# Optimization experiments

Measured on AMD Instinct MI355X. Metric: run time of the kernel, lower is better.

Reference implementation:

```python
import jax, jax.numpy as jnp
import numpy as np

LOSS_WEIGHT = 1.0
EPS = 1e-12  # numerical floor under the sqrt (module's eps)


def setup_inputs() -> dict:
    key = jax.random.key(0)
    k1, k2 = jax.random.split(key)
    N, P1, P2, D = 16, 4096, 4096, 2
    point_set_1 = jax.random.normal(k1, (N, P1, D), dtype=jnp.float32)
    point_set_2 = jax.random.normal(k2, (N, P2, D), dtype=jnp.float32)
    return {"point_set_1": point_set_1, "point_set_2": point_set_2}


def _chamfer_per_object(x, y):
    # x: [N, P1, 2], y: [N, P2, 2]
    # Pairwise squared L2 via expansion |x|^2 + |y|^2 - 2<x,y> (avoids [N,P1,P2,2] diff tensor)
    x2 = jnp.sum(x * x, axis=-1)                       # [N, P1]
    y2 = jnp.sum(y * y, axis=-1)                       # [N, P2]
    xy = jnp.einsum('npd,nqd->npq', x, y)              # [N, P1, P2]
    C = jnp.sqrt(jnp.clip(x2[:, :, None] + y2[:, None, :] - 2.0 * xy, EPS))  # [N, P1, P2]
    d1 = jnp.min(C, axis=-1).mean(axis=-1)             # min over P2, mean over P1 -> [N]
    d2 = jnp.min(C, axis=-2).mean(axis=-1)             # min over P1, mean over P2 -> [N]
    return 0.5 * (d1 + d2)                             # [N]


def reference(point_set_1, point_set_2):
    # Vectorized form of the per-object Python loop:
    # each object's chamfer (reduction='mean' over a batch of 1 == identity)
    # is masked by (set_2.sum() >= 0), summed, and divided by n_obj.
    cost = _chamfer_per_object(point_set_1, point_set_2)                 # [N]
    m = (jnp.sum(point_set_2, axis=(-1, -2)) >= 0).astype(cost.dtype)    # [N]
    return jnp.mean(cost * m) * LOSS_WEIGHT                              # scalar
```

## Files before the change

kernel.cpp:

```cpp
#include <hip/hip_runtime.h>
#include <math.h>

typedef float f32x2 __attribute__((ext_vector_type(2)));

#define N_OBJ 16
#define P 4096
#define BLOCK 256
#define R 8
#define ROWS_PER_BLOCK (BLOCK * R)
#define ROWBLOCKS (P / ROWS_PER_BLOCK)
#define CQ 16
#define QCHUNK (P / CQ)
#define JP (QCHUNK / 2)
#define EPSF 1e-12f
#define GRID_MAIN (2 * N_OBJ * ROWBLOCKS * CQ)

#define RED_ROWS 1024
#define RED_SLICES (P / RED_ROWS)
#define GRID_RED (2 * N_OBJ * RED_SLICES)


__device__ __forceinline__ float wave_sum(float s) {
#pragma unroll
    for (int off = 32; off > 0; off >>= 1)
        s += __shfl_xor(s, off, 64);
    return s;
}

__global__ __launch_bounds__(BLOCK) void k_main(const float* __restrict__ s1,
                                                const float* __restrict__ s2,
                                                float* __restrict__ pmin,
                                                unsigned* __restrict__ maskws) {
    const int per_pass = N_OBJ * ROWBLOCKS * CQ;
    int bid  = blockIdx.x;
    int tid  = threadIdx.x;
    int pass = bid / per_pass;
    int idx  = bid % per_pass;
    int n    = idx / (ROWBLOCKS * CQ);
    int rem  = idx % (ROWBLOCKS * CQ);
    int rb   = rem / CQ;
    int cq   = rem % CQ;

    __shared__ float4 lds[JP];
    __shared__ float wpart[BLOCK / 64];

    const float* T = (pass == 0) ? s1 : s2;
    const float* S = (pass == 0) ? s2 : s1;

    if (tid < JP) {
        int q = cq * QCHUNK + 2 * tid;
        float4 v = ((const float4*)S)[(n * P + q) >> 1];
        lds[tid] = make_float4(v.x, v.z, v.y, v.w);
    }

    f32x2 a0s[R], a1s[R];
    float c[R], m[R];
    int rbase = rb * ROWS_PER_BLOCK;
#pragma unroll
    for (int k = 0; k < R; k++) {
        int r = rbase + k * BLOCK + tid;
        float2 x = ((const float2*)T)[n * P + r];
        float a0 = -2.0f * x.x, a1 = -2.0f * x.y;
        a0s[k] = (f32x2){a0, a0};
        a1s[k] = (f32x2){a1, a1};
        c[k]   = fmaf(x.x, x.x, x.y * x.y);
        m[k]   = INFINITY;
    }

    {
        const float4* v2 = (const float4*)s2;
        float s = 0.0f;
#pragma unroll
        for (int k = 0; k < 8; k++) {
            float4 v = v2[n * 2048 + k * BLOCK + tid];
            s += (v.x + v.y) + (v.z + v.w);
        }
        s = wave_sum(s);
        if ((tid & 63) == 0) wpart[tid >> 6] = s;
    }
    __syncthreads();
    float total = (wpart[0] + wpart[1]) + (wpart[2] + wpart[3]);
    unsigned live = (total >= 0.0f) ? 1u : 0u;
    if (pass == 0 && rem == 0 && tid == 0) maskws[n] = live;
    if (!live) return;

#pragma unroll 4
    for (int jp = 0; jp < JP; jp++) {
        float4 v = lds[jp];
        f32x2 y0 = {v.x, v.y};
        f32x2 y1 = {v.z, v.w};
        f32x2 y2 = y0 * y0 + y1 * y1;
#pragma unroll
        for (int k = 0; k < R; k++) {
            f32x2 t = a1s[k] * y1 + y2;
            f32x2 d = a0s[k] * y0 + t;
            m[k] = fminf(fminf(d.x, d.y), m[k]);
        }
    }

    float* outp = pmin + ((size_t)((pass * N_OBJ + n) * CQ + cq)) * P
                + rbase + tid;
#pragma unroll
    for (int k = 0; k < R; k++) {
        outp[k * BLOCK] = fmaxf(m[k] + c[k], EPSF);
    }
}

__global__ __launch_bounds__(BLOCK) void k_red(const float* __restrict__ pmin,
                                               const unsigned* __restrict__ maskws,
                                               float* __restrict__ out) {
    int bid = blockIdx.x;
    int tid = threadIdx.x;
    int pn  = bid / RED_SLICES;
    int rs  = bid % RED_SLICES;
    int n   = pn & (N_OBJ - 1);
    __shared__ float wpart[BLOCK / 64];

    if (maskws[n] == 0u) return;

    const float* base = pmin + (size_t)pn * CQ * P + rs * RED_ROWS + 4 * tid;
    float4 mn = make_float4(INFINITY, INFINITY, INFINITY, INFINITY);
#pragma unroll
    for (int cq = 0; cq < CQ; cq++) {
        float4 v = *(const float4*)(base + (size_t)cq * P);
        mn.x = fminf(mn.x, v.x);
        mn.y = fminf(mn.y, v.y);
        mn.z = fminf(mn.z, v.z);
        mn.w = fminf(mn.w, v.w);
    }
    float s = (sqrtf(mn.x) + sqrtf(mn.y)) + (sqrtf(mn.z) + sqrtf(mn.w));
    s = wave_sum(s);
    if ((tid & 63) == 0) wpart[tid >> 6] = s;
    __syncthreads();
    if (tid == 0) {
        float sum = (wpart[0] + wpart[1]) + (wpart[2] + wpart[3]);
        atomicAdd(out, sum * (0.5f / (float)P / (float)N_OBJ));
    }
}

extern "C" void kernel_launch(void* const* d_in, const int* in_sizes, int n_in,
                              void* d_out, int out_size, void* d_ws, size_t ws_size,
                              hipStream_t stream) {
    const float* s1 = (const float*)d_in[0];
    const float* s2 = (const float*)d_in[1];
    float* out = (float*)d_out;

    float* pmin = (float*)d_ws;
    unsigned* maskws = (unsigned*)(pmin + 2 * N_OBJ * CQ * P);

    k_main<<<GRID_MAIN, BLOCK, 0, stream>>>(s1, s2, pmin, maskws);
    k_red<<<GRID_RED, BLOCK, 0, stream>>>(pmin, maskws, out);
}
```

Measured before the change: 86.90 us.

## Replace brute-force pairwise min with uniform-grid nearest-neighbor search

Instead of computing all P1×P2 distances, each point set is bucketed into a 96×96 uniform grid using a counting sort in LDS, one block per set. Queries then search rings of cells outward from their own cell and stop once the ring distance exceeds the current best. This removes the quadratic compute and the partial-min reduction pass. In exchange it adds a build kernel with only 32 blocks, data-dependent divergent loops, and a fixed grid range of [-6, 6] with edge clamping. Out-of-range points are clamped into edge cells, so the ring-termination bound may not hold for them and results could differ for inputs far outside that range.

```diff
diff --git a/kernel.cpp b/kernel.cpp
--- a/kernel.cpp
+++ b/kernel.cpp
@@ -1,23 +1,19 @@
 #include <hip/hip_runtime.h>
 #include <math.h>
-
-typedef float f32x2 __attribute__((ext_vector_type(2)));
 
 #define N_OBJ 16
 #define P 4096
 #define BLOCK 256
-#define R 8
-#define ROWS_PER_BLOCK (BLOCK * R)
-#define ROWBLOCKS (P / ROWS_PER_BLOCK)
-#define CQ 16
-#define QCHUNK (P / CQ)
-#define JP (QCHUNK / 2)
 #define EPSF 1e-12f
-#define GRID_MAIN (2 * N_OBJ * ROWBLOCKS * CQ)
-
-#define RED_ROWS 1024
-#define RED_SLICES (P / RED_ROWS)
-#define GRID_RED (2 * N_OBJ * RED_SLICES)
+
+#define G 96
+#define GG (G * G)
+#define NGRID (2 * N_OBJ)
+#define LO (-6.0f)
+#define CELL 0.125f
+#define INV_CELL 8.0f
+#define BPT (GG / BLOCK)
+#define QBLOCKS (2 * N_OBJ * (P / BLOCK))
 
 
 __device__ __forceinline__ float wave_sum(float s) {
@@ -27,113 +23,164 @@
     return s;
 }
 
-__global__ __launch_bounds__(BLOCK) void k_main(const float* __restrict__ s1,
-                                                const float* __restrict__ s2,
-                                                float* __restrict__ pmin,
-                                                unsigned* __restrict__ maskws) {
-    const int per_pass = N_OBJ * ROWBLOCKS * CQ;
+__global__ __launch_bounds__(BLOCK) void k_build(const float* __restrict__ s1,
+                                                 const float* __restrict__ s2,
+                                                 float2* __restrict__ pts,
+                                                 unsigned* __restrict__ binStart,
+                                                 unsigned* __restrict__ maskws) {
+    int gid = blockIdx.x;
+    int n = gid >> 1, t = gid & 1;
+    int tid = threadIdx.x;
+    const float2* src = (const float2*)(t ? s1 : s2) + n * P;
+
+    __shared__ unsigned cnt[GG];
+    __shared__ unsigned scanbuf[BLOCK];
+    __shared__ float wq[BLOCK / 64];
+
+    for (int i = tid; i < GG; i += BLOCK) cnt[i] = 0u;
+    __syncthreads();
+
+    float2 p[16];
+    int b[16];
+    float msum = 0.0f;
+#pragma unroll
+    for (int k = 0; k < 16; k++) {
+        float2 v = src[k * BLOCK + tid];
+        p[k] = v;
+        msum += v.x + v.y;
+        int bx = (int)((v.x - LO) * INV_CELL);
+        int by = (int)((v.y - LO) * INV_CELL);
+        bx = min(max(bx, 0), G - 1);
+        by = min(max(by, 0), G - 1);
+        b[k] = by * G + bx;
+        atomicAdd(&cnt[b[k]], 1u);
+    }
+    msum = wave_sum(msum);
+    if ((tid & 63) == 0) wq[tid >> 6] = msum;
+    __syncthreads();
+    if (t == 0 && tid == 0) {
+        float total = (wq[0] + wq[1]) + (wq[2] + wq[3]);
+        maskws[n] = (total >= 0.0f) ? 1u : 0u;
+    }
+
+    unsigned run = 0;
+    int base = tid * BPT;
+    for (int i = 0; i < BPT; i++) {
+        unsigned cv = cnt[base + i];
+        cnt[base + i] = run;
+        run += cv;
+    }
+    scanbuf[tid] = run;
+    __syncthreads();
+    for (int d = 1; d < BLOCK; d <<= 1) {
+        unsigned v = (tid >= d) ? scanbuf[tid - d] : 0u;
+        __syncthreads();
+        scanbuf[tid] += v;
+        __syncthreads();
+    }
+    unsigned offs = scanbuf[tid] - run;
+    for (int i = 0; i < BPT; i++) cnt[base + i] += offs;
+    __syncthreads();
+
+    unsigned* bs = binStart + (size_t)gid * (GG + 1);
+    for (int i = tid; i < GG; i += BLOCK) bs[i] = cnt[i];
+    if (tid == 0) bs[GG] = P;
+    __syncthreads();
+
+    float2* dst = pts + (size_t)gid * P;
+#pragma unroll
+    for (int k = 0; k < 16; k++) {
+        unsigned idx = atomicAdd(&cnt[b[k]], 1u);
+        dst[idx] = p[k];
+    }
+}
+
+__global__ __launch_bounds__(BLOCK) void k_query(const float2* __restrict__ pts,
+                                                 const unsigned* __restrict__ binStart,
+                                                 const unsigned* __restrict__ maskws,
+                                                 float* __restrict__ out) {
     int bid  = blockIdx.x;
     int tid  = threadIdx.x;
-    int pass = bid / per_pass;
-    int idx  = bid % per_pass;
-    int n    = idx / (ROWBLOCKS * CQ);
-    int rem  = idx % (ROWBLOCKS * CQ);
-    int rb   = rem / CQ;
-    int cq   = rem % CQ;
-
-    __shared__ float4 lds[JP];
-    __shared__ float wpart[BLOCK / 64];
-
-    const float* T = (pass == 0) ? s1 : s2;
-    const float* S = (pass == 0) ? s2 : s1;
-
-    if (tid < JP) {
-        int q = cq * QCHUNK + 2 * tid;
-        float4 v = ((const float4*)S)[(n * P + q) >> 1];
-        lds[tid] = make_float4(v.x, v.z, v.y, v.w);
-    }
-
-    f32x2 a0s[R], a1s[R];
-    float c[R], m[R];
-    int rbase = rb * ROWS_PER_BLOCK;
-#pragma unroll
-    for (int k = 0; k < R; k++) {
-        int r = rbase + k * BLOCK + tid;
-        float2 x = ((const float2*)T)[n * P + r];
-        float a0 = -2.0f * x.x, a1 = -2.0f * x.y;
-        a0s[k] = (f32x2){a0, a0};
-        a1s[k] = (f32x2){a1, a1};
-        c[k]   = fmaf(x.x, x.x, x.y * x.y);
-        m[k]   = INFINITY;
-    }
-
-    {
-        const float4* v2 = (const float4*)s2;
-        float s = 0.0f;
-#pragma unroll
-        for (int k = 0; k < 8; k++) {
-            float4 v = v2[n * 2048 + k * BLOCK + tid];
-            s += (v.x + v.y) + (v.z + v.w);
-        }
-        s = wave_sum(s);
-        if ((tid & 63) == 0) wpart[tid >> 6] = s;
-    }
-    __syncthreads();
-    float total = (wpart[0] + wpart[1]) + (wpart[2] + wpart[3]);
-    unsigned live = (total >= 0.0f) ? 1u : 0u;
-    if (pass == 0 && rem == 0 && tid == 0) maskws[n] = live;
-    if (!live) return;
-
-#pragma unroll 4
-    for (int jp = 0; jp < JP; jp++) {
-        float4 v = lds[jp];
-        f32x2 y0 = {v.x, v.y};
-        f32x2 y1 = {v.z, v.w};
-        f32x2 y2 = y0 * y0 + y1 * y1;
-#pragma unroll
-        for (int k = 0; k < R; k++) {
-            f32x2 t = a1s[k] * y1 + y2;
-            f32x2 d = a0s[k] * y0 + t;
-            m[k] = fminf(fminf(d.x, d.y), m[k]);
-        }
-    }
-
-    float* outp = pmin + ((size_t)((pass * N_OBJ + n) * CQ + cq)) * P
-                + rbase + tid;
-#pragma unroll
-    for (int k = 0; k < R; k++) {
-        outp[k * BLOCK] = fmaxf(m[k] + c[k], EPSF);
-    }
-}
-
-__global__ __launch_bounds__(BLOCK) void k_red(const float* __restrict__ pmin,
-                                               const unsigned* __restrict__ maskws,
-                                               float* __restrict__ out) {
-    int bid = blockIdx.x;
-    int tid = threadIdx.x;
-    int pn  = bid / RED_SLICES;
-    int rs  = bid % RED_SLICES;
-    int n   = pn & (N_OBJ - 1);
-    __shared__ float wpart[BLOCK / 64];
+    int pass = bid >> 8;
+    int rem  = bid & 255;
+    int n    = rem >> 4;
+    int qc   = rem & 15;
+    __shared__ float wq[BLOCK / 64];
 
     if (maskws[n] == 0u) return;
 
-    const float* base = pmin + (size_t)pn * CQ * P + rs * RED_ROWS + 4 * tid;
-    float4 mn = make_float4(INFINITY, INFINITY, INFINITY, INFINITY);
-#pragma unroll
-    for (int cq = 0; cq < CQ; cq++) {
-        float4 v = *(const float4*)(base + (size_t)cq * P);
-        mn.x = fminf(mn.x, v.x);
-        mn.y = fminf(mn.y, v.y);
-        mn.z = fminf(mn.z, v.z);
-        mn.w = fminf(mn.w, v.w);
-    }
-    float s = (sqrtf(mn.x) + sqrtf(mn.y)) + (sqrtf(mn.z) + sqrtf(mn.w));
-    s = wave_sum(s);
-    if ((tid & 63) == 0) wpart[tid >> 6] = s;
+    int g_tgt = n * 2 + pass;
+    int g_src = n * 2 + (1 - pass);
+    const float2* tp   = pts + (size_t)g_tgt * P;
+    const unsigned* bs = binStart + (size_t)g_tgt * (GG + 1);
+
+    float2 q = pts[(size_t)g_src * P + qc * BLOCK + tid];
+    float c   = fmaf(q.x, q.x, q.y * q.y);
+    float nqx = -2.0f * q.x, nqy = -2.0f * q.y;
+    int bx = min(max((int)((q.x - LO) * INV_CELL), 0), G - 1);
+    int by = min(max((int)((q.y - LO) * INV_CELL), 0), G - 1);
+
+    float m = INFINITY;
+    for (int r = 0; r <= 2 * G; r++) {
+        if (r >= 2) {
+            float bb = (float)(r - 1) * CELL;
+            if (bb * bb > m + c) break;
+        }
+        int xs = max(bx - r, 0), xe = min(bx + r, G - 1);
+        int ylo = by - r, yhi = by + r;
+        if (ylo >= 0) {
+            unsigned s = bs[ylo * G + xs], e = bs[ylo * G + xe + 1];
+            for (unsigned i = s; i < e; i++) {
+                float2 y = tp[i];
+                float y2 = fmaf(y.x, y.x, y.y * y.y);
+                float d  = fmaf(nqy, y.y, y2);
+                d = fmaf(nqx, y.x, d);
+                m = fminf(m, d);
+            }
+        }
+        if (r > 0 && yhi <= G - 1) {
+            unsigned s = bs[yhi * G + xs], e = bs[yhi * G + xe + 1];
+            for (unsigned i = s; i < e; i++) {
+                float2 y = tp[i];
+                float y2 = fmaf(y.x, y.x, y.y * y.y);
+                float d  = fmaf(nqy, y.y, y2);
+                d = fmaf(nqx, y.x, d);
+                m = fminf(m, d);
+            }
+        }
+        if (r > 0) {
+            int ya = max(ylo + 1, 0), yb = min(yhi - 1, G - 1);
+            for (int y = ya; y <= yb; y++) {
+                if (bx - r >= 0) {
+                    unsigned s = bs[y * G + bx - r], e = bs[y * G + bx - r + 1];
+                    for (unsigned i = s; i < e; i++) {
+                        float2 yy = tp[i];
+                        float y2 = fmaf(yy.x, yy.x, yy.y * yy.y);
+                        float d  = fmaf(nqy, yy.y, y2);
+                        d = fmaf(nqx, yy.x, d);
+                        m = fminf(m, d);
+                    }
+                }
+                if (bx + r <= G - 1) {
+                    unsigned s = bs[y * G + bx + r], e = bs[y * G + bx + r + 1];
+                    for (unsigned i = s; i < e; i++) {
+                        float2 yy = tp[i];
+                        float y2 = fmaf(yy.x, yy.x, yy.y * yy.y);
+                        float d  = fmaf(nqy, yy.y, y2);
+                        d = fmaf(nqx, yy.x, d);
+                        m = fminf(m, d);
+                    }
+                }
+            }
+        }
+    }
+
+    float dq = sqrtf(fmaxf(m + c, EPSF));
+    dq = wave_sum(dq);
+    if ((tid & 63) == 0) wq[tid >> 6] = dq;
     __syncthreads();
     if (tid == 0) {
-        float sum = (wpart[0] + wpart[1]) + (wpart[2] + wpart[3]);
+        float sum = (wq[0] + wq[1]) + (wq[2] + wq[3]);
         atomicAdd(out, sum * (0.5f / (float)P / (float)N_OBJ));
     }
 }
@@ -145,9 +192,10 @@
     const float* s2 = (const float*)d_in[1];
     float* out = (float*)d_out;
 
-    float* pmin = (float*)d_ws;
-    unsigned* maskws = (unsigned*)(pmin + 2 * N_OBJ * CQ * P);
-
-    k_main<<<GRID_MAIN, BLOCK, 0, stream>>>(s1, s2, pmin, maskws);
-    k_red<<<GRID_RED, BLOCK, 0, stream>>>(pmin, maskws, out);
-}
+    float2* pts        = (float2*)d_ws;
+    unsigned* binStart = (unsigned*)(pts + NGRID * P);
+    unsigned* maskws   = binStart + NGRID * (GG + 1);
+
+    k_build<<<NGRID, BLOCK, 0, stream>>>(s1, s2, pts, binStart, maskws);
+    k_query<<<QBLOCKS, BLOCK, 0, stream>>>(pts, binStart, maskws, out);
+}
```

Measured after the change: 119.1 us. +37.1%, slower.
